# Kernel tuning notes

Measured on AMD Instinct MI355X. Metric: run time of the kernel, lower is better.

## Reference

```python
import jax, jax.numpy as jnp
import numpy as np

B, S, D = 2, 512, 128      # batch, seq_len, d_att
DG, NG = 64, 2             # d_group, n_group = D // DG


def setup_inputs() -> dict:
    key = jax.random.key(0)
    ks = jax.random.split(key, 12)
    def w(k, shape, scale):
        return jax.random.normal(k, shape, dtype=jnp.float32) * scale
    proj_scale = 1.0 / D                      # xavier_uniform-ish std / sqrt(d_att)
    mlp1 = (2.0 / (DG + DG)) ** 0.5
    mlp2 = (2.0 / (DG + 16)) ** 0.5
    mlp3 = (2.0 / (16 + 1)) ** 0.5
    return {
        "x": w(ks[0], (B, S, D), 1.0),
        "positional_adding_bias": w(ks[1], (1, NG, 1, S, S), 1.0),
        "positional_multiplying_bias": jax.random.uniform(ks[2], (1, NG, 1, S, S), dtype=jnp.float32),
        "Wq": w(ks[3], (D, D), proj_scale),
        "Wk": w(ks[4], (D, D), proj_scale),
        "Wv": w(ks[5], (D, D), proj_scale),
        "W1": w(ks[6], (DG, DG), mlp1), "b1": jnp.zeros((DG,), jnp.float32),
        "W2": w(ks[7], (DG, 16), mlp2), "b2": jnp.zeros((16,), jnp.float32),
        "W3": w(ks[8], (16, 1), mlp3),  "b3": jnp.zeros((1,), jnp.float32),
    }


def reference(x, positional_adding_bias, positional_multiplying_bias,
              Wq, Wk, Wv, W1, b1, W2, b2, W3, b3):
    Q = x @ Wq   # [B,S,D]
    K = x @ Wk
    V = x @ Wv
    # pairwise Q-K differences, grouped: [B,S,S,NG,DG] (d_att split as n_group,d_group)
    diff = (Q[:, :, None, :] - K[:, None, :, :]).reshape(B, S, S, NG, DG)
    # per-group scoring MLP (Linear->ReLU x3, final width 1)
    h = jax.nn.relu(diff @ W1 + b1)
    h = jax.nn.relu(h @ W2 + b2)
    a = jax.nn.relu(h @ W3 + b3)                 # [B,S,S,NG,1]
    a = jnp.transpose(a, (0, 3, 4, 1, 2))        # [B,NG,1,S,S]
    a = a * positional_multiplying_bias + positional_adding_bias
    a = jax.nn.softmax(a, axis=-1)[:, :, 0]      # [B,NG,S,S], softmax over keys
    # NOTE: original reshapes V as (d_group, n_group) — faithful reproduction
    Vr = V.reshape(B, S, DG, NG)                 # [B,S,DG,NG]
    out = jnp.einsum('bisk,bkji->bsji', a, Vr)   # [B,S,DG,NG]
    return out.reshape(B, S, D)
```

## Files before the change

### kernel.cpp

```cpp
#include <hip/hip_runtime.h>

#define BQ 2
#define SQ 512
#define DQ 128
#define DGQ 64
#define NGQ 2


__global__ __launch_bounds__(256) void fuse_w_kernel(
    const float* __restrict__ Wq, const float* __restrict__ Wk,
    const float* __restrict__ W1,
    float* __restrict__ Wq1, float* __restrict__ Wk1)
{
    const int id = blockIdx.x * 256 + threadIdx.x;
    const int which = id >> 14;
    const int rem = id & 16383;
    const int d = rem >> 7;
    const int f = rem & 127;
    const int g = f >> 6, c = f & 63;
    const float* W = which ? Wk : Wq;
    float acc = 0.f;
    #pragma unroll 8
    for (int e = 0; e < DGQ; ++e)
        acc = fmaf(W[d * DQ + g * DGQ + e], W1[e * DGQ + c], acc);
    (which ? Wk1 : Wq1)[d * DQ + f] = acc;
}

__global__ __launch_bounds__(256) void proj_kernel(
    const float* __restrict__ x,
    const float* __restrict__ Wq1, const float* __restrict__ Wk1,
    const float* __restrict__ Wv, const float* __restrict__ b1,
    float* __restrict__ QW1, float* __restrict__ KW1, float* __restrict__ Vp)
{
    const int t = threadIdx.x;
    const int f = t & 127, h = t >> 7;
    const int row = blockIdx.x;
    __shared__ float xs[DQ];
    __shared__ float part[3][2][DQ];

    if (t < DQ) xs[t] = x[(size_t)row * DQ + t];
    __syncthreads();

    float aq = 0.f, ak = 0.f, av = 0.f;
    const int d0 = h * 64;
    #pragma unroll 8
    for (int d = 0; d < 64; ++d) {
        const float xv = xs[d0 + d];
        aq = fmaf(xv, Wq1[(size_t)(d0 + d) * DQ + f], aq);
        ak = fmaf(xv, Wk1[(size_t)(d0 + d) * DQ + f], ak);
        av = fmaf(xv, Wv [(size_t)(d0 + d) * DQ + f], av);
    }
    part[0][h][f] = aq; part[1][h][f] = ak; part[2][h][f] = av;
    __syncthreads();

    if (h == 0) {
        QW1[(size_t)row * DQ + f] = aq + part[0][1][f] + b1[f & 63];
        KW1[(size_t)row * DQ + f] = ak + part[1][1][f];
    } else {
        const float v = part[2][0][f] + av;
        Vp[((size_t)row * NGQ + (f & 1)) * DGQ + (f >> 1)] = v;
    }
}

__global__ __launch_bounds__(512) void attn_kernel(
    const float* __restrict__ QW1, const float* __restrict__ KW1,
    const float* __restrict__ Vp,
    const float* __restrict__ W2, const float* __restrict__ b2,
    const float* __restrict__ W3, const float* __restrict__ b3,
    const float* __restrict__ pos_add, const float* __restrict__ pos_mul,
    float* __restrict__ out)
{
    const int t = threadIdx.x;
    const int i = blockIdx.x & (SQ - 1);
    const int g = (blockIdx.x >> 9) & 1;
    const int b = blockIdx.x >> 10;

    __shared__ float qs[DGQ];
    __shared__ float scores[SQ];
    __shared__ float red[8];
    __shared__ float av[8][DGQ];

    if (t < DGQ) qs[t] = QW1[((size_t)(b * SQ + i)) * DQ + g * DGQ + t];
    const size_t biasoff = ((size_t)g * SQ + i) * SQ + t;
    const float pmv = pos_mul[biasoff];
    const float pav = pos_add[biasoff];
    __syncthreads();

    const float4* krow = reinterpret_cast<const float4*>(
        KW1 + ((size_t)(b * SQ + t)) * DQ + g * DGQ);

    float acc[16];
    #pragma unroll
    for (int o = 0; o < 16; ++o) acc[o] = b2[o];

    #pragma unroll 2
    for (int c4 = 0; c4 < 16; ++c4) {
        const float4 kv = krow[c4];
        const float q0 = qs[c4 * 4 + 0], q1 = qs[c4 * 4 + 1];
        const float q2 = qs[c4 * 4 + 2], q3 = qs[c4 * 4 + 3];
        const float h0 = fmaxf(q0 - kv.x, 0.f);
        const float h1 = fmaxf(q1 - kv.y, 0.f);
        const float h2 = fmaxf(q2 - kv.z, 0.f);
        const float h3 = fmaxf(q3 - kv.w, 0.f);
        const float* w2r = W2 + c4 * 64;
        #pragma unroll
        for (int o = 0; o < 16; ++o) {
            acc[o] = fmaf(h0, w2r[o],      acc[o]);
            acc[o] = fmaf(h1, w2r[16 + o], acc[o]);
            acc[o] = fmaf(h2, w2r[32 + o], acc[o]);
            acc[o] = fmaf(h3, w2r[48 + o], acc[o]);
        }
    }
    float a = b3[0];
    #pragma unroll
    for (int o = 0; o < 16; ++o) a = fmaf(fmaxf(acc[o], 0.f), W3[o], a);
    a = fmaxf(a, 0.f);
    const float logit = fmaf(a, pmv, pav);

    float m = logit;
    #pragma unroll
    for (int off = 32; off > 0; off >>= 1) m = fmaxf(m, __shfl_xor(m, off));
    const int wave = t >> 6;
    if ((t & 63) == 0) red[wave] = m;
    __syncthreads();
    m = fmaxf(fmaxf(fmaxf(red[0], red[1]), fmaxf(red[2], red[3])),
              fmaxf(fmaxf(red[4], red[5]), fmaxf(red[6], red[7])));
    const float e = __expf(logit - m);
    scores[t] = e;
    float s = e;
    #pragma unroll
    for (int off = 32; off > 0; off >>= 1) s += __shfl_xor(s, off);
    __syncthreads();
    if ((t & 63) == 0) red[wave] = s;
    __syncthreads();
    const float inv = 1.f / (red[0] + red[1] + red[2] + red[3] +
                             red[4] + red[5] + red[6] + red[7]);

    const int dim = t & 63, q = t >> 6;
    const float* vbase = Vp + (((size_t)(b * SQ + q * 64)) * NGQ + g) * DGQ + dim;
    float accv = 0.f;
    #pragma unroll 4
    for (int k = 0; k < 64; ++k)
        accv = fmaf(scores[q * 64 + k], vbase[(size_t)k * (NGQ * DGQ)], accv);
    av[q][dim] = accv;
    __syncthreads();
    if (t < DGQ) {
        float sum = 0.f;
        #pragma unroll
        for (int q2 = 0; q2 < 8; ++q2) sum += av[q2][t];
        out[((size_t)(b * SQ + i)) * DQ + t * NGQ + g] = sum * inv;
    }
}

extern "C" void kernel_launch(void* const* d_in, const int* in_sizes, int n_in,
                              void* d_out, int out_size, void* d_ws, size_t ws_size,
                              hipStream_t stream) {
    const float* x       = (const float*)d_in[0];
    const float* pos_add = (const float*)d_in[1];
    const float* pos_mul = (const float*)d_in[2];
    const float* Wq      = (const float*)d_in[3];
    const float* Wk      = (const float*)d_in[4];
    const float* Wv      = (const float*)d_in[5];
    const float* W1      = (const float*)d_in[6];
    const float* b1      = (const float*)d_in[7];
    const float* W2      = (const float*)d_in[8];
    const float* b2      = (const float*)d_in[9];
    const float* W3      = (const float*)d_in[10];
    const float* b3      = (const float*)d_in[11];
    float* out = (float*)d_out;

    float* ws  = (float*)d_ws;
    float* Wq1 = ws;
    float* Wk1 = ws + 16384;
    float* QW1 = ws + 32768;
    float* KW1 = ws + 163840;
    float* Vp  = ws + 294912;

    fuse_w_kernel<<<128, 256, 0, stream>>>(Wq, Wk, W1, Wq1, Wk1);
    proj_kernel<<<BQ * SQ, 256, 0, stream>>>(x, Wq1, Wk1, Wv, b1, QW1, KW1, Vp);
    attn_kernel<<<BQ * NGQ * SQ, 512, 0, stream>>>(QW1, KW1, Vp, W2, b2, W3, b3,
                                                   pos_add, pos_mul, out);
}
```

Measured before the change: 137.8 us.

## Process two query rows per attention block and fold W1 into projection kernel

The attention kernel now handles two query rows per block, so each loaded K row, W2 weight and V value serves two queries. The MLP uses packed float2 math and the softmax reductions run for both rows together. The separate weight-fusion kernel is removed: the projection kernel computes Q and K and then applies W1 itself, which drops one launch. The trade-off is more registers per thread and half as many attention blocks.

Result: faster. 129.6 us (-6.0%).

```diff
diff --git a/kernel.cpp b/kernel.cpp
--- a/kernel.cpp
+++ b/kernel.cpp
@@ -6,60 +6,57 @@
 #define DGQ 64
 #define NGQ 2
 
-
-__global__ __launch_bounds__(256) void fuse_w_kernel(
-    const float* __restrict__ Wq, const float* __restrict__ Wk,
-    const float* __restrict__ W1,
-    float* __restrict__ Wq1, float* __restrict__ Wk1)
-{
-    const int id = blockIdx.x * 256 + threadIdx.x;
-    const int which = id >> 14;
-    const int rem = id & 16383;
-    const int d = rem >> 7;
-    const int f = rem & 127;
-    const int g = f >> 6, c = f & 63;
-    const float* W = which ? Wk : Wq;
-    float acc = 0.f;
-    #pragma unroll 8
-    for (int e = 0; e < DGQ; ++e)
-        acc = fmaf(W[d * DQ + g * DGQ + e], W1[e * DGQ + c], acc);
-    (which ? Wk1 : Wq1)[d * DQ + f] = acc;
-}
+typedef float float2v __attribute__((ext_vector_type(2)));
+
 
 __global__ __launch_bounds__(256) void proj_kernel(
     const float* __restrict__ x,
-    const float* __restrict__ Wq1, const float* __restrict__ Wk1,
-    const float* __restrict__ Wv, const float* __restrict__ b1,
+    const float* __restrict__ Wq, const float* __restrict__ Wk,
+    const float* __restrict__ Wv,
+    const float* __restrict__ W1, const float* __restrict__ b1,
     float* __restrict__ QW1, float* __restrict__ KW1, float* __restrict__ Vp)
 {
     const int t = threadIdx.x;
-    const int f = t & 127, h = t >> 7;
     const int row = blockIdx.x;
     __shared__ float xs[DQ];
     __shared__ float part[3][2][DQ];
+    __shared__ float qs[DQ], ks[DQ];
 
     if (t < DQ) xs[t] = x[(size_t)row * DQ + t];
     __syncthreads();
 
+    const int f = t & 127, h = t >> 7;
     float aq = 0.f, ak = 0.f, av = 0.f;
     const int d0 = h * 64;
     #pragma unroll 8
     for (int d = 0; d < 64; ++d) {
         const float xv = xs[d0 + d];
-        aq = fmaf(xv, Wq1[(size_t)(d0 + d) * DQ + f], aq);
-        ak = fmaf(xv, Wk1[(size_t)(d0 + d) * DQ + f], ak);
-        av = fmaf(xv, Wv [(size_t)(d0 + d) * DQ + f], av);
+        const size_t o = (size_t)(d0 + d) * DQ + f;
+        aq = fmaf(xv, Wq[o], aq);
+        ak = fmaf(xv, Wk[o], ak);
+        av = fmaf(xv, Wv[o], av);
     }
     part[0][h][f] = aq; part[1][h][f] = ak; part[2][h][f] = av;
     __syncthreads();
 
-    if (h == 0) {
-        QW1[(size_t)row * DQ + f] = aq + part[0][1][f] + b1[f & 63];
-        KW1[(size_t)row * DQ + f] = ak + part[1][1][f];
+    if (t < DQ) {
+        qs[t] = part[0][0][t] + part[0][1][t];
+        const float v = part[2][0][t] + part[2][1][t];
+        Vp[((size_t)row * NGQ + (t & 1)) * DGQ + (t >> 1)] = v;
     } else {
-        const float v = part[2][0][f] + av;
-        Vp[((size_t)row * NGQ + (f & 1)) * DGQ + (f >> 1)] = v;
-    }
+        const int f2 = t - DQ;
+        ks[f2] = part[1][0][f2] + part[1][1][f2];
+    }
+    __syncthreads();
+
+    const int fb = t & 127, side = t >> 7;
+    const int g = fb >> 6, c = fb & 63;
+    const float* src = side ? ks : qs;
+    float acc = side ? 0.f : b1[c];
+    #pragma unroll 8
+    for (int e = 0; e < 64; ++e)
+        acc = fmaf(src[g * 64 + e], W1[e * DGQ + c], acc);
+    (side ? KW1 : QW1)[(size_t)row * DQ + fb] = acc;
 }
 
 __global__ __launch_bounds__(512) void attn_kernel(
@@ -71,84 +68,116 @@
     float* __restrict__ out)
 {
     const int t = threadIdx.x;
-    const int i = blockIdx.x & (SQ - 1);
-    const int g = (blockIdx.x >> 9) & 1;
-    const int b = blockIdx.x >> 10;
-
-    __shared__ float qs[DGQ];
-    __shared__ float scores[SQ];
-    __shared__ float red[8];
-    __shared__ float av[8][DGQ];
-
-    if (t < DGQ) qs[t] = QW1[((size_t)(b * SQ + i)) * DQ + g * DGQ + t];
-    const size_t biasoff = ((size_t)g * SQ + i) * SQ + t;
-    const float pmv = pos_mul[biasoff];
-    const float pav = pos_add[biasoff];
+    const int ipair = blockIdx.x & 255;
+    const int g = (blockIdx.x >> 8) & 1;
+    const int b = blockIdx.x >> 9;
+    const int i0 = ipair * 2;
+
+    __shared__ __align__(16) float qsl[2][DGQ];
+    __shared__ __align__(8)  float sc[SQ * 2];
+    __shared__ float redm[2][8], reds[2][8];
+    __shared__ float avs[2][8][DGQ];
+
+    if (t < 2 * DGQ) {
+        const int qq = t >> 6, e = t & 63;
+        qsl[qq][e] = QW1[((size_t)(b * SQ + i0 + qq)) * DQ + g * DGQ + e];
+    }
+    const size_t bo0 = ((size_t)g * SQ + i0) * SQ + t;
+    const float pm0 = pos_mul[bo0],      pa0 = pos_add[bo0];
+    const float pm1 = pos_mul[bo0 + SQ], pa1 = pos_add[bo0 + SQ];
     __syncthreads();
 
     const float4* krow = reinterpret_cast<const float4*>(
         KW1 + ((size_t)(b * SQ + t)) * DQ + g * DGQ);
-
-    float acc[16];
-    #pragma unroll
-    for (int o = 0; o < 16; ++o) acc[o] = b2[o];
+    const float2v* qv0 = reinterpret_cast<const float2v*>(&qsl[0][0]);
+    const float2v* qv1 = reinterpret_cast<const float2v*>(&qsl[1][0]);
+    const float2v* b2v = reinterpret_cast<const float2v*>(b2);
+
+    float2v acc0[8], acc1[8];
+    #pragma unroll
+    for (int o = 0; o < 8; ++o) { acc0[o] = b2v[o]; acc1[o] = b2v[o]; }
 
     #pragma unroll 2
     for (int c4 = 0; c4 < 16; ++c4) {
         const float4 kv = krow[c4];
-        const float q0 = qs[c4 * 4 + 0], q1 = qs[c4 * 4 + 1];
-        const float q2 = qs[c4 * 4 + 2], q3 = qs[c4 * 4 + 3];
-        const float h0 = fmaxf(q0 - kv.x, 0.f);
-        const float h1 = fmaxf(q1 - kv.y, 0.f);
-        const float h2 = fmaxf(q2 - kv.z, 0.f);
-        const float h3 = fmaxf(q3 - kv.w, 0.f);
-        const float* w2r = W2 + c4 * 64;
+        const float2v k01 = {kv.x, kv.y}, k23 = {kv.z, kv.w};
+        const float2v d01a = qv0[c4 * 2] - k01,     d23a = qv0[c4 * 2 + 1] - k23;
+        const float2v d01b = qv1[c4 * 2] - k01,     d23b = qv1[c4 * 2 + 1] - k23;
+        const float ha0 = fmaxf(d01a.x, 0.f), ha1 = fmaxf(d01a.y, 0.f);
+        const float ha2 = fmaxf(d23a.x, 0.f), ha3 = fmaxf(d23a.y, 0.f);
+        const float hb0 = fmaxf(d01b.x, 0.f), hb1 = fmaxf(d01b.y, 0.f);
+        const float hb2 = fmaxf(d23b.x, 0.f), hb3 = fmaxf(d23b.y, 0.f);
+        const float2v* w2r = reinterpret_cast<const float2v*>(W2 + c4 * 64);
         #pragma unroll
-        for (int o = 0; o < 16; ++o) {
-            acc[o] = fmaf(h0, w2r[o],      acc[o]);
-            acc[o] = fmaf(h1, w2r[16 + o], acc[o]);
-            acc[o] = fmaf(h2, w2r[32 + o], acc[o]);
-            acc[o] = fmaf(h3, w2r[48 + o], acc[o]);
+        for (int o = 0; o < 8; ++o) {
+            const float2v w0 = w2r[o], w1 = w2r[8 + o];
+            const float2v w2_ = w2r[16 + o], w3_ = w2r[24 + o];
+            acc0[o] += ha0 * w0;  acc0[o] += ha1 * w1;
+            acc0[o] += ha2 * w2_; acc0[o] += ha3 * w3_;
+            acc1[o] += hb0 * w0;  acc1[o] += hb1 * w1;
+            acc1[o] += hb2 * w2_; acc1[o] += hb3 * w3_;
         }
     }
-    float a = b3[0];
-    #pragma unroll
-    for (int o = 0; o < 16; ++o) a = fmaf(fmaxf(acc[o], 0.f), W3[o], a);
-    a = fmaxf(a, 0.f);
-    const float logit = fmaf(a, pmv, pav);
-
-    float m = logit;
-    #pragma unroll
-    for (int off = 32; off > 0; off >>= 1) m = fmaxf(m, __shfl_xor(m, off));
+    float a0 = b3[0], a1 = b3[0];
+    #pragma unroll
+    for (int o = 0; o < 8; ++o) {
+        a0 = fmaf(fmaxf(acc0[o].x, 0.f), W3[2 * o], a0);
+        a0 = fmaf(fmaxf(acc0[o].y, 0.f), W3[2 * o + 1], a0);
+        a1 = fmaf(fmaxf(acc1[o].x, 0.f), W3[2 * o], a1);
+        a1 = fmaf(fmaxf(acc1[o].y, 0.f), W3[2 * o + 1], a1);
+    }
+    const float logit0 = fmaf(fmaxf(a0, 0.f), pm0, pa0);
+    const float logit1 = fmaf(fmaxf(a1, 0.f), pm1, pa1);
+
+    float m0 = logit0, m1 = logit1;
+    #pragma unroll
+    for (int off = 32; off > 0; off >>= 1) {
+        m0 = fmaxf(m0, __shfl_xor(m0, off));
+        m1 = fmaxf(m1, __shfl_xor(m1, off));
+    }
     const int wave = t >> 6;
-    if ((t & 63) == 0) red[wave] = m;
-    __syncthreads();
-    m = fmaxf(fmaxf(fmaxf(red[0], red[1]), fmaxf(red[2], red[3])),
-              fmaxf(fmaxf(red[4], red[5]), fmaxf(red[6], red[7])));
-    const float e = __expf(logit - m);
-    scores[t] = e;
-    float s = e;
-    #pragma unroll
-    for (int off = 32; off > 0; off >>= 1) s += __shfl_xor(s, off);
-    __syncthreads();
-    if ((t & 63) == 0) red[wave] = s;
-    __syncthreads();
-    const float inv = 1.f / (red[0] + red[1] + red[2] + red[3] +
-                             red[4] + red[5] + red[6] + red[7]);
+    if ((t & 63) == 0) { redm[0][wave] = m0; redm[1][wave] = m1; }
+    __syncthreads();
+    float M0 = redm[0][0], M1 = redm[1][0];
+    #pragma unroll
+    for (int w = 1; w < 8; ++w) {
+        M0 = fmaxf(M0, redm[0][w]); M1 = fmaxf(M1, redm[1][w]);
+    }
+    const float e0 = __expf(logit0 - M0);
+    const float e1 = __expf(logit1 - M1);
+    *reinterpret_cast<float2v*>(&sc[t * 2]) = float2v{e0, e1};
+    float s0 = e0, s1 = e1;
+    #pragma unroll
+    for (int off = 32; off > 0; off >>= 1) {
+        s0 += __shfl_xor(s0, off);
+        s1 += __shfl_xor(s1, off);
+    }
+    if ((t & 63) == 0) { reds[0][wave] = s0; reds[1][wave] = s1; }
+    __syncthreads();
+    float S0 = 0.f, S1 = 0.f;
+    #pragma unroll
+    for (int w = 0; w < 8; ++w) { S0 += reds[0][w]; S1 += reds[1][w]; }
+    const float inv0 = 1.f / S0, inv1 = 1.f / S1;
 
     const int dim = t & 63, q = t >> 6;
     const float* vbase = Vp + (((size_t)(b * SQ + q * 64)) * NGQ + g) * DGQ + dim;
-    float accv = 0.f;
-    #pragma unroll 4
-    for (int k = 0; k < 64; ++k)
-        accv = fmaf(scores[q * 64 + k], vbase[(size_t)k * (NGQ * DGQ)], accv);
-    av[q][dim] = accv;
-    __syncthreads();
-    if (t < DGQ) {
+    float2v accv = {0.f, 0.f};
+    #pragma unroll 8
+    for (int k = 0; k < 64; ++k) {
+        const float v = vbase[(size_t)k * (NGQ * DGQ)];
+        const float2v sv = *reinterpret_cast<const float2v*>(&sc[(q * 64 + k) * 2]);
+        accv += v * sv;
+    }
+    avs[0][q][dim] = accv.x;
+    avs[1][q][dim] = accv.y;
+    __syncthreads();
+    if (t < 2 * DGQ) {
+        const int qq = t >> 6, d = t & 63;
         float sum = 0.f;
         #pragma unroll
-        for (int q2 = 0; q2 < 8; ++q2) sum += av[q2][t];
-        out[((size_t)(b * SQ + i)) * DQ + t * NGQ + g] = sum * inv;
+        for (int w = 0; w < 8; ++w) sum += avs[qq][w][d];
+        out[((size_t)(b * SQ + i0 + qq)) * DQ + d * NGQ + g] =
+            sum * (qq ? inv1 : inv0);
     }
 }
 
@@ -170,14 +199,13 @@
     float* out = (float*)d_out;
 
     float* ws  = (float*)d_ws;
-    float* Wq1 = ws;
-    float* Wk1 = ws + 16384;
-    float* QW1 = ws + 32768;
-    float* KW1 = ws + 163840;
-    float* Vp  = ws + 294912;
-
-    fuse_w_kernel<<<128, 256, 0, stream>>>(Wq, Wk, W1, Wq1, Wk1);
-    proj_kernel<<<BQ * SQ, 256, 0, stream>>>(x, Wq1, Wk1, Wv, b1, QW1, KW1, Vp);
-    attn_kernel<<<BQ * NGQ * SQ, 512, 0, stream>>>(QW1, KW1, Vp, W2, b2, W3, b3,
-                                                   pos_add, pos_mul, out);
+    float* QW1 = ws;
+    float* KW1 = ws + 131072;
+    float* Vp  = ws + 262144;
+
+    proj_kernel<<<BQ * SQ, 256, 0, stream>>>(x, Wq, Wk, Wv, W1, b1,
+                                             QW1, KW1, Vp);
+    attn_kernel<<<BQ * NGQ * SQ / 2, 512, 0, stream>>>(QW1, KW1, Vp, W2, b2,
+                                                       W3, b3, pos_add, pos_mul,
+                                                       out);
 }
```
